# Optimization experiments

Hardware: AMD Instinct MI355X
Metric: run time of the kernel (lower is better)

The kernel has to match this reference:

```python
import jax, jax.numpy as jnp
import numpy as np

B, L, D = 2, 384, 128
N, DHS, DHP = 8, 16, 4  # heads, scalar head dim, point head dim
D_SCALAR = N * DHS          # 128
D_POINT = N * DHP * 3       # 96
D_OUT_IN = D_SCALAR + D * N + D_POINT + N * DHP  # 1280


def setup_inputs() -> dict:
    key = jax.random.key(0)
    ks = jax.random.split(key, 14)
    sc = 0.05
    x = jax.random.normal(ks[0], (B, L, D), dtype=jnp.float32)
    e = jax.random.normal(ks[1], (B, L, L, D), dtype=jnp.float32)
    r = jax.random.normal(ks[2], (B, L, 3, 3), dtype=jnp.float32)
    t = jax.random.normal(ks[3], (B, L, 3), dtype=jnp.float32)
    Wq_s = jax.random.normal(ks[4], (D, D_SCALAR)) * sc
    Wk_s = jax.random.normal(ks[5], (D, D_SCALAR)) * sc
    Wv_s = jax.random.normal(ks[6], (D, D_SCALAR)) * sc
    Wb = jax.random.normal(ks[7], (D, N)) * sc
    Wq_p = jax.random.normal(ks[8], (D, D_POINT)) * sc
    Wk_p = jax.random.normal(ks[9], (D, D_POINT)) * sc
    Wv_p = jax.random.normal(ks[10], (D, D_POINT)) * sc
    gamma = jnp.full((N,), float(np.log(np.exp(1.0) - 1.0)), dtype=jnp.float32)
    Wo = jax.random.normal(ks[11], (D_OUT_IN, D)) * sc
    bo = jnp.zeros((D,), dtype=jnp.float32)
    return {"x": x, "e": e, "r": r, "t": t, "Wq_s": Wq_s, "Wk_s": Wk_s,
            "Wv_s": Wv_s, "Wb": Wb, "Wq_p": Wq_p, "Wk_p": Wk_p,
            "Wv_p": Wv_p, "gamma": gamma, "Wo": Wo, "bo": bo}


def _heads_scalar(y):  # (b,l,n*d) -> (b,n,l,d)
    b, l, _ = y.shape
    return y.reshape(b, l, N, DHS).transpose(0, 2, 1, 3)


def _heads_point(y):  # (b,l,n*p*3) -> (b,n,l,p,3)
    b, l, _ = y.shape
    return y.reshape(b, l, N, DHP, 3).transpose(0, 2, 1, 3, 4)


def reference(x, e, r, t, Wq_s, Wk_s, Wv_s, Wb, Wq_p, Wk_p, Wv_p, gamma, Wo, bo):
    b, l, _ = x.shape
    qs = _heads_scalar(x @ Wq_s)
    ks_ = _heads_scalar(x @ Wk_s)
    vs = _heads_scalar(x @ Wv_s)

    # local points -> global frame: x_row @ r + t (note row-vector convention)
    t_b = t[:, None, :, None, :]  # (b,1,l,1,3)
    qp = jnp.einsum('bnlpk,blkc->bnlpc', _heads_point(x @ Wq_p), r) + t_b
    kp = jnp.einsum('bnlpk,blkc->bnlpc', _heads_point(x @ Wk_p), r) + t_b
    vp = jnp.einsum('bnlpk,blkc->bnlpc', _heads_point(x @ Wv_p), r) + t_b

    logit_scalar = jnp.einsum('bnid,bnjd->bnij', qs, ks_) * (DHS ** -0.5)
    bias_pair = jnp.einsum('bijd,dn->bnij', e, Wb)

    # sum_{p,c} (q_i - k_j)^2 via norm expansion (same math, no O(l^2 p 3) tensor)
    qq = jnp.sum(qp * qp, axis=(-1, -2))  # (b,n,i)
    kk = jnp.sum(kp * kp, axis=(-1, -2))  # (b,n,j)
    cross = jnp.einsum('bnipc,bnjpc->bnij', qp, kp)
    dist2 = qq[..., :, None] + kk[..., None, :] - 2.0 * cross
    logit_point = (-0.5 * 0.25) * gamma[None, :, None, None] * dist2

    logit = (3.0 ** -0.5) * (logit_scalar + bias_pair + logit_point)
    attn = jax.nn.softmax(logit, axis=-1)  # (b,n,i,j)

    out_scalar = jnp.einsum('bnij,bnjd->bnid', attn, vs)
    out_scalar = out_scalar.transpose(0, 2, 1, 3).reshape(b, l, N * DHS)

    out_pair = jnp.einsum('bnij,bijd->bnid', attn, e)
    out_pair = out_pair.transpose(0, 2, 1, 3).reshape(b, l, N * D)

    op = jnp.einsum('bnij,bnjpc->bnipc', attn, vp)
    # inverse transform: (x - t) @ r^T  -> out[c] = sum_k (x-t)[k] * r[c,k]
    op_local = jnp.einsum('bnipk,bick->bnipc', op - t_b, r)
    op_norm = jnp.linalg.norm(op_local, axis=-1)  # (b,n,i,p)

    out_point = op_local.transpose(0, 2, 1, 3, 4).reshape(b, l, N * DHP * 3)
    out_norm = op_norm.transpose(0, 2, 1, 3).reshape(b, l, N * DHP)

    out = jnp.concatenate([out_scalar, out_pair, out_point, out_norm], axis=-1)
    return out @ Wo + bo
```

## Files before the change

kernel.cpp:

```cpp
#include <hip/hip_runtime.h>

#define LL 384
#define NH 8

typedef const float* fp32p;

__global__ __launch_bounds__(128) void k_proj(
    fp32p x, fp32p r, fp32p tvec,
    fp32p Wqs, fp32p Wks, fp32p Wvs,
    fp32p Wqp, fp32p Wkp, fp32p Wvp,
    float* qs, float* ks, float* vs,
    float* qp, float* kp, float* vp)
{
  int bl = blockIdx.x;
  int t = threadIdx.x;
  __shared__ float xs[128];
  __shared__ float yq[96], yk[96], yv[96];
  xs[t] = x[bl*128 + t];
  __syncthreads();
  float aq = 0.f, ak = 0.f, av = 0.f;
  #pragma unroll 4
  for (int d = 0; d < 128; ++d) {
    float xv = xs[d];
    aq += xv * Wqs[d*128 + t];
    ak += xv * Wks[d*128 + t];
    av += xv * Wvs[d*128 + t];
  }
  int b = bl / LL, l = bl - (bl / LL) * LL;
  int n = t >> 4, dhs = t & 15;
  int rowbase = (b*NH + n)*LL + l;
  qs[rowbase*16 + dhs] = aq;
  ks[rowbase*16 + dhs] = ak;
  vs[rowbase*16 + dhs] = av;
  if (t < 96) {
    float pq = 0.f, pk = 0.f, pv = 0.f;
    #pragma unroll 4
    for (int d = 0; d < 128; ++d) {
      float xv = xs[d];
      pq += xv * Wqp[d*96 + t];
      pk += xv * Wkp[d*96 + t];
      pv += xv * Wvp[d*96 + t];
    }
    yq[t] = pq; yk[t] = pk; yv[t] = pv;
  }
  __syncthreads();
  if (t < 96) {
    int np = t / 12;
    int rem = t - np*12;
    int p = rem / 3, c = rem - p*3;
    float rr0 = r[(bl*3 + 0)*3 + c];
    float rr1 = r[(bl*3 + 1)*3 + c];
    float rr2 = r[(bl*3 + 2)*3 + c];
    float tt  = tvec[bl*3 + c];
    int base = np*12 + p*3;
    int prow = (b*NH + np)*LL + l;
    qp[prow*12 + p*3 + c] = yq[base]*rr0 + yq[base+1]*rr1 + yq[base+2]*rr2 + tt;
    kp[prow*12 + p*3 + c] = yk[base]*rr0 + yk[base+1]*rr1 + yk[base+2]*rr2 + tt;
    vp[prow*12 + p*3 + c] = yv[base]*rr0 + yv[base+1]*rr1 + yv[base+2]*rr2 + tt;
  }
}

__global__ __launch_bounds__(256) void k_fused(
    fp32p e, fp32p Wb, fp32p gamma, fp32p r, fp32p tvec,
    const float* qs, const float* ks, const float* vs,
    const float* qp, const float* kp, const float* vp,
    float* cat)
{
  int bi = blockIdx.x;
  int b = bi / LL, i = bi - (bi / LL)*LL;
  int t = threadIdx.x;
  __shared__ float attnS[8*385];
  __shared__ float WbS[1024];
  __shared__ float qS[128];
  __shared__ float qpS[96];
  __shared__ float qqS[8], coefS[8];
  __shared__ float redS[128*9];
  __shared__ float opS[96];

  const float* ebase = e + (size_t)bi*LL*128;

  #pragma unroll
  for (int u = 0; u < 4; ++u) WbS[t + u*256] = Wb[t + u*256];
  if (t < 128) {
    int n = t >> 4, d = t & 15;
    qS[t] = qs[(size_t)(((b*NH + n)*LL + i))*16 + d];
  } else if (t < 224) {
    int tt = t - 128;
    int n = tt / 12, d = tt - n*12;
    qpS[tt] = qp[(size_t)(((b*NH + n)*LL + i))*12 + d];
  } else if (t < 232) {
    coefS[t - 224] = -0.125f * gamma[t - 224];
  }
  __syncthreads();

  if (t < 192) {
    const float4* er0 = reinterpret_cast<const float4*>(ebase + (size_t)t*128);
    const float4* er1 = reinterpret_cast<const float4*>(ebase + (size_t)(t + 192)*128);
    float acc0[8] = {0,0,0,0,0,0,0,0};
    float acc1[8] = {0,0,0,0,0,0,0,0};
    for (int d4 = 0; d4 < 32; ++d4) {
      float4 e0 = er0[d4], e1 = er1[d4];
      float a0[4] = {e0.x, e0.y, e0.z, e0.w};
      float a1[4] = {e1.x, e1.y, e1.z, e1.w};
      #pragma unroll
      for (int k = 0; k < 4; ++k) {
        int d = d4*4 + k;
        float4 w0 = *reinterpret_cast<const float4*>(&WbS[d*8]);
        float4 w1 = *reinterpret_cast<const float4*>(&WbS[d*8 + 4]);
        acc0[0] += a0[k]*w0.x; acc0[1] += a0[k]*w0.y; acc0[2] += a0[k]*w0.z; acc0[3] += a0[k]*w0.w;
        acc0[4] += a0[k]*w1.x; acc0[5] += a0[k]*w1.y; acc0[6] += a0[k]*w1.z; acc0[7] += a0[k]*w1.w;
        acc1[0] += a1[k]*w0.x; acc1[1] += a1[k]*w0.y; acc1[2] += a1[k]*w0.z; acc1[3] += a1[k]*w0.w;
        acc1[4] += a1[k]*w1.x; acc1[5] += a1[k]*w1.y; acc1[6] += a1[k]*w1.z; acc1[7] += a1[k]*w1.w;
      }
    }
    #pragma unroll
    for (int n = 0; n < 8; ++n) {
      attnS[n*385 + t]       = acc0[n];
      attnS[n*385 + t + 192] = acc1[n];
    }
  } else if (t < 200) {
    int n = t - 192;
    float s = 0.f;
    #pragma unroll
    for (int k = 0; k < 12; ++k) { float v = qpS[n*12 + k]; s += v*v; }
    qqS[n] = s;
  }
  __syncthreads();

  if (t < 192) {
    #pragma unroll
    for (int n = 0; n < 8; ++n) {
      int bn = b*NH + n;
      float4 q0 = *reinterpret_cast<const float4*>(&qS[n*16]);
      float4 q1 = *reinterpret_cast<const float4*>(&qS[n*16 + 4]);
      float4 q2 = *reinterpret_cast<const float4*>(&qS[n*16 + 8]);
      float4 q3 = *reinterpret_cast<const float4*>(&qS[n*16 + 12]);
      float4 p0 = *reinterpret_cast<const float4*>(&qpS[n*12]);
      float4 p1 = *reinterpret_cast<const float4*>(&qpS[n*12 + 4]);
      float4 p2 = *reinterpret_cast<const float4*>(&qpS[n*12 + 8]);
      float qq = qqS[n], coef = coefS[n];
      #pragma unroll
      for (int jj = 0; jj < 2; ++jj) {
        int j = t + jj*192;
        size_t rowk = (size_t)bn*LL + j;
        const float4* k4  = reinterpret_cast<const float4*>(ks + rowk*16);
        const float4* kp4 = reinterpret_cast<const float4*>(kp + rowk*12);
        float4 k0 = k4[0], k1 = k4[1], k2 = k4[2], k3 = k4[3];
        float dots = q0.x*k0.x + q0.y*k0.y + q0.z*k0.z + q0.w*k0.w
                   + q1.x*k1.x + q1.y*k1.y + q1.z*k1.z + q1.w*k1.w
                   + q2.x*k2.x + q2.y*k2.y + q2.z*k2.z + q2.w*k2.w
                   + q3.x*k3.x + q3.y*k3.y + q3.z*k3.z + q3.w*k3.w;
        float4 c0 = kp4[0], c1 = kp4[1], c2 = kp4[2];
        float cross = p0.x*c0.x + p0.y*c0.y + p0.z*c0.z + p0.w*c0.w
                    + p1.x*c1.x + p1.y*c1.y + p1.z*c1.z + p1.w*c1.w
                    + p2.x*c2.x + p2.y*c2.y + p2.z*c2.z + p2.w*c2.w;
        float kk = c0.x*c0.x + c0.y*c0.y + c0.z*c0.z + c0.w*c0.w
                 + c1.x*c1.x + c1.y*c1.y + c1.z*c1.z + c1.w*c1.w
                 + c2.x*c2.x + c2.y*c2.y + c2.z*c2.z + c2.w*c2.w;
        float bs = attnS[n*385 + j];
        attnS[n*385 + j] = 0.57735027f * (0.25f*dots + bs + coef*(qq + kk - 2.f*cross));
      }
    }
  }
  __syncthreads();

  {
    int wv = t >> 6, lane = t & 63;
    #pragma unroll
    for (int nn2 = 0; nn2 < 2; ++nn2) {
      int n = wv*2 + nn2;
      float v[6];
      #pragma unroll
      for (int q = 0; q < 6; ++q) v[q] = attnS[n*385 + lane + q*64];
      float m = v[0];
      #pragma unroll
      for (int q = 1; q < 6; ++q) m = fmaxf(m, v[q]);
      #pragma unroll
      for (int off = 32; off >= 1; off >>= 1) m = fmaxf(m, __shfl_xor(m, off, 64));
      float s = 0.f;
      #pragma unroll
      for (int q = 0; q < 6; ++q) { v[q] = __expf(v[q] - m); s += v[q]; }
      #pragma unroll
      for (int off = 32; off >= 1; off >>= 1) s += __shfl_xor(s, off, 64);
      float inv = 1.f / s;
      #pragma unroll
      for (int q = 0; q < 6; ++q) attnS[n*385 + lane + q*64] = v[q]*inv;
    }
  }
  __syncthreads();

  if (t < 224) {
    int n = t / 28, d = t - (t / 28)*28;
    const float* an = attnS + n*385;
    size_t rowbase = (size_t)(b*NH + n)*LL;
    float acc = 0.f;
    if (d < 16) {
      const float* src = vs + rowbase*16 + d;
      for (int j = 0; j < LL; ++j) acc += an[j] * src[j*16];
      cat[(size_t)bi*1280 + n*16 + d] = acc;
    } else {
      const float* src = vp + rowbase*12 + (d - 16);
      for (int j = 0; j < LL; ++j) acc += an[j] * src[j*12];
      opS[n*12 + (d - 16)] = acc;
    }
  }
  __syncthreads();

  {
    int oct = t & 15, n3 = (t >> 4) & 7, half = t >> 7;
    const float* an = attnS + n3*385;
    const float4* e4 = reinterpret_cast<const float4*>(ebase);
    float acc[8] = {0,0,0,0,0,0,0,0};
    for (int jj = 0; jj < 192; ++jj) {
      int j = 2*jj + half;
      float4 va = e4[j*32 + oct*2];
      float4 vb = e4[j*32 + oct*2 + 1];
      float a = an[j];
      acc[0] += a*va.x; acc[1] += a*va.y; acc[2] += a*va.z; acc[3] += a*va.w;
      acc[4] += a*vb.x; acc[5] += a*vb.y; acc[6] += a*vb.z; acc[7] += a*vb.w;
    }
    if (half) {
      #pragma unroll
      for (int k = 0; k < 8; ++k) redS[(t - 128)*9 + k] = acc[k];
    }
    __syncthreads();
    if (!half) {
      float* dst = cat + (size_t)bi*1280 + 128 + n3*128 + oct*8;
      #pragma unroll
      for (int k = 0; k < 8; ++k) dst[k] = acc[k] + redS[t*9 + k];
    }
  }

  if (t < 32) {
    int n = t >> 2, p = t & 3;
    float o[3];
    #pragma unroll
    for (int k = 0; k < 3; ++k) o[k] = opS[n*12 + p*3 + k] - tvec[bi*3 + k];
    float loc[3];
    #pragma unroll
    for (int c = 0; c < 3; ++c) {
      float s = 0.f;
      #pragma unroll
      for (int k = 0; k < 3; ++k) s += o[k] * r[(bi*3 + c)*3 + k];
      loc[c] = s;
    }
    float* dst = cat + (size_t)bi*1280;
    dst[1152 + n*12 + p*3 + 0] = loc[0];
    dst[1152 + n*12 + p*3 + 1] = loc[1];
    dst[1152 + n*12 + p*3 + 2] = loc[2];
    dst[1248 + n*4 + p] = sqrtf(loc[0]*loc[0] + loc[1]*loc[1] + loc[2]*loc[2]);
  }
}

__global__ __launch_bounds__(256) void k_out(const float* cat, fp32p Wo, fp32p bo,
                                             float* out)
{
  int r0 = blockIdx.x * 8;
  int t = threadIdx.x;
  __shared__ float catS[8*1280];
  {
    const float4* c4 = reinterpret_cast<const float4*>(cat + (size_t)r0*1280);
    float4* s4 = reinterpret_cast<float4*>(catS);
    for (int idx = t; idx < 2560; idx += 256) s4[idx] = c4[idx];
  }
  __syncthreads();
  int row = t >> 5;
  int cg  = t & 31;
  const float* crow = catS + row*1280;
  const float4* w4 = reinterpret_cast<const float4*>(Wo) + cg;
  float ax = 0.f, ay = 0.f, az = 0.f, aw = 0.f;
  for (int k = 0; k < 1280; k += 16) {
    float4 w[16]; float a[16];
    #pragma unroll
    for (int u = 0; u < 16; ++u) { w[u] = w4[(k + u)*32]; a[u] = crow[k + u]; }
    #pragma unroll
    for (int u = 0; u < 16; ++u) {
      ax += a[u]*w[u].x; ay += a[u]*w[u].y; az += a[u]*w[u].z; aw += a[u]*w[u].w;
    }
  }
  float4 bv = reinterpret_cast<const float4*>(bo)[cg];
  float4 res = { ax + bv.x, ay + bv.y, az + bv.z, aw + bv.w };
  reinterpret_cast<float4*>(out + (size_t)(r0 + row)*128)[cg] = res;
}

extern "C" void kernel_launch(void* const* d_in, const int* in_sizes, int n_in,
                              void* d_out, int out_size, void* d_ws, size_t ws_size,
                              hipStream_t stream)
{
  fp32p x    = (fp32p)d_in[0];
  fp32p e    = (fp32p)d_in[1];
  fp32p r    = (fp32p)d_in[2];
  fp32p tv   = (fp32p)d_in[3];
  fp32p Wqs  = (fp32p)d_in[4];
  fp32p Wks  = (fp32p)d_in[5];
  fp32p Wvs  = (fp32p)d_in[6];
  fp32p Wb   = (fp32p)d_in[7];
  fp32p Wqp  = (fp32p)d_in[8];
  fp32p Wkp  = (fp32p)d_in[9];
  fp32p Wvp  = (fp32p)d_in[10];
  fp32p gam  = (fp32p)d_in[11];
  fp32p Wo   = (fp32p)d_in[12];
  fp32p bo   = (fp32p)d_in[13];
  float* out = (float*)d_out;

  float* qs  = (float*)d_ws;
  float* ks  = qs + 98304;
  float* vs  = ks + 98304;
  float* qp  = vs + 98304;
  float* kp  = qp + 73728;
  float* vp  = kp + 73728;
  float* cat = vp + 73728;

  k_proj<<<768, 128, 0, stream>>>(x, r, tv, Wqs, Wks, Wvs, Wqp, Wkp, Wvp,
                                  qs, ks, vs, qp, kp, vp);
  k_fused<<<768, 256, 0, stream>>>(e, Wb, gam, r, tv, qs, ks, vs, qp, kp, vp, cat);
  k_out<<<96, 256, 0, stream>>>(cat, Wo, bo, out);
}
```

Measured before the change: 439.7 us.

## Split fused attention kernel into logit, softmax, AV, pair and point kernels

The monolithic per-row kernel is broken into separate kernels for the logits, softmax, attention-times-values, the pair aggregation over the edge tensor, and the point back-transform. Attention weights now round-trip through a global buffer, and the pair aggregation is split four ways along j, with results combined by atomic adds into a pre-zeroed output buffer. The aim is more parallelism and occupancy than 768 heavy blocks using large shared memory could offer. The cost is extra launches, about 9 MB of attention-matrix traffic and float atomics, while the 75 MB edge tensor is still read twice.

```diff
diff --git a/kernel.cpp b/kernel.cpp
--- a/kernel.cpp
+++ b/kernel.cpp
@@ -4,6 +4,11 @@
 #define NH 8
 
 typedef const float* fp32p;
+
+__global__ __launch_bounds__(256) void k_zero(float4* p)
+{
+  p[(size_t)blockIdx.x*256 + threadIdx.x] = make_float4(0.f, 0.f, 0.f, 0.f);
+}
 
 __global__ __launch_bounds__(128) void k_proj(
     fp32p x, fp32p r, fp32p tvec,
@@ -19,7 +24,6 @@
   xs[t] = x[bl*128 + t];
   __syncthreads();
   float aq = 0.f, ak = 0.f, av = 0.f;
-  #pragma unroll 4
   for (int d = 0; d < 128; ++d) {
     float xv = xs[d];
     aq += xv * Wqs[d*128 + t];
@@ -34,7 +38,6 @@
   vs[rowbase*16 + dhs] = av;
   if (t < 96) {
     float pq = 0.f, pk = 0.f, pv = 0.f;
-    #pragma unroll 4
     for (int d = 0; d < 128; ++d) {
       float xv = xs[d];
       pq += xv * Wqp[d*96 + t];
@@ -60,196 +63,174 @@
   }
 }
 
-__global__ __launch_bounds__(256) void k_fused(
-    fp32p e, fp32p Wb, fp32p gamma, fp32p r, fp32p tvec,
-    const float* qs, const float* ks, const float* vs,
-    const float* qp, const float* kp, const float* vp,
-    float* cat)
-{
-  int bi = blockIdx.x;
+__global__ __launch_bounds__(256) void k_logit(
+    fp32p e, fp32p Wb, fp32p gamma,
+    const float* qs, const float* ks, const float* qp, const float* kp,
+    float* attn)
+{
+  __shared__ float WbS[1024];
+  int t = threadIdx.x;
+  #pragma unroll
+  for (int u = 0; u < 4; ++u) WbS[t + u*256] = Wb[t + u*256];
+  __syncthreads();
+  int gtid = blockIdx.x*256 + t;
+  int bi = gtid / 192, j0 = gtid - (gtid / 192)*192;
+  int b = bi / LL, i = bi - (bi / LL)*LL;
+  const float4* er0 = reinterpret_cast<const float4*>(e + ((size_t)bi*LL + j0)*128);
+  const float4* er1 = reinterpret_cast<const float4*>(e + ((size_t)bi*LL + j0 + 192)*128);
+  float acc0[8] = {0,0,0,0,0,0,0,0};
+  float acc1[8] = {0,0,0,0,0,0,0,0};
+  for (int d4 = 0; d4 < 32; ++d4) {
+    float4 e0 = er0[d4], e1 = er1[d4];
+    float a0[4] = {e0.x, e0.y, e0.z, e0.w};
+    float a1[4] = {e1.x, e1.y, e1.z, e1.w};
+    #pragma unroll
+    for (int k = 0; k < 4; ++k) {
+      int d = d4*4 + k;
+      float4 w0 = *reinterpret_cast<const float4*>(&WbS[d*8]);
+      float4 w1 = *reinterpret_cast<const float4*>(&WbS[d*8 + 4]);
+      acc0[0] += a0[k]*w0.x; acc0[1] += a0[k]*w0.y; acc0[2] += a0[k]*w0.z; acc0[3] += a0[k]*w0.w;
+      acc0[4] += a0[k]*w1.x; acc0[5] += a0[k]*w1.y; acc0[6] += a0[k]*w1.z; acc0[7] += a0[k]*w1.w;
+      acc1[0] += a1[k]*w0.x; acc1[1] += a1[k]*w0.y; acc1[2] += a1[k]*w0.z; acc1[3] += a1[k]*w0.w;
+      acc1[4] += a1[k]*w1.x; acc1[5] += a1[k]*w1.y; acc1[6] += a1[k]*w1.z; acc1[7] += a1[k]*w1.w;
+    }
+  }
+  #pragma unroll
+  for (int n = 0; n < 8; ++n) {
+    size_t rq = (size_t)(b*NH + n)*LL + i;
+    const float4* q4 = reinterpret_cast<const float4*>(qs + rq*16);
+    float4 q0 = q4[0], q1 = q4[1], q2 = q4[2], q3 = q4[3];
+    const float4* p4 = reinterpret_cast<const float4*>(qp + rq*12);
+    float4 p0 = p4[0], p1 = p4[1], p2 = p4[2];
+    float qq = p0.x*p0.x + p0.y*p0.y + p0.z*p0.z + p0.w*p0.w
+             + p1.x*p1.x + p1.y*p1.y + p1.z*p1.z + p1.w*p1.w
+             + p2.x*p2.x + p2.y*p2.y + p2.z*p2.z + p2.w*p2.w;
+    float coef = -0.125f * gamma[n];
+    #pragma unroll
+    for (int jj = 0; jj < 2; ++jj) {
+      int j = j0 + jj*192;
+      size_t rk = (size_t)(b*NH + n)*LL + j;
+      const float4* k4  = reinterpret_cast<const float4*>(ks + rk*16);
+      const float4* kp4 = reinterpret_cast<const float4*>(kp + rk*12);
+      float4 k0 = k4[0], k1 = k4[1], k2 = k4[2], k3 = k4[3];
+      float dots = q0.x*k0.x + q0.y*k0.y + q0.z*k0.z + q0.w*k0.w
+                 + q1.x*k1.x + q1.y*k1.y + q1.z*k1.z + q1.w*k1.w
+                 + q2.x*k2.x + q2.y*k2.y + q2.z*k2.z + q2.w*k2.w
+                 + q3.x*k3.x + q3.y*k3.y + q3.z*k3.z + q3.w*k3.w;
+      float4 c0 = kp4[0], c1 = kp4[1], c2 = kp4[2];
+      float cross = p0.x*c0.x + p0.y*c0.y + p0.z*c0.z + p0.w*c0.w
+                  + p1.x*c1.x + p1.y*c1.y + p1.z*c1.z + p1.w*c1.w
+                  + p2.x*c2.x + p2.y*c2.y + p2.z*c2.z + p2.w*c2.w;
+      float kk = c0.x*c0.x + c0.y*c0.y + c0.z*c0.z + c0.w*c0.w
+               + c1.x*c1.x + c1.y*c1.y + c1.z*c1.z + c1.w*c1.w
+               + c2.x*c2.x + c2.y*c2.y + c2.z*c2.z + c2.w*c2.w;
+      float bias = jj ? acc1[n] : acc0[n];
+      attn[((size_t)(b*NH + n)*LL + i)*LL + j] =
+          0.57735027f * (0.25f*dots + bias + coef*(qq + kk - 2.f*cross));
+    }
+  }
+}
+
+__global__ __launch_bounds__(256) void k_soft(float* attn)
+{
+  int row = blockIdx.x*4 + (threadIdx.x >> 6);
+  int lane = threadIdx.x & 63;
+  float* arow = attn + (size_t)row*LL;
+  float v[6];
+  #pragma unroll
+  for (int q = 0; q < 6; ++q) v[q] = arow[lane + q*64];
+  float m = v[0];
+  #pragma unroll
+  for (int q = 1; q < 6; ++q) m = fmaxf(m, v[q]);
+  #pragma unroll
+  for (int off = 32; off >= 1; off >>= 1) m = fmaxf(m, __shfl_xor(m, off, 64));
+  float s = 0.f;
+  #pragma unroll
+  for (int q = 0; q < 6; ++q) { v[q] = __expf(v[q] - m); s += v[q]; }
+  #pragma unroll
+  for (int off = 32; off >= 1; off >>= 1) s += __shfl_xor(s, off, 64);
+  float inv = 1.f / s;
+  #pragma unroll
+  for (int q = 0; q < 6; ++q) arow[lane + q*64] = v[q]*inv;
+}
+
+__global__ __launch_bounds__(256) void k_av(
+    const float* attn, const float* vs, const float* vp, float* cat, float* opb)
+{
+  int tid = blockIdx.x*256 + threadIdx.x;
+  int row = tid >> 5;
+  int dim = tid & 31;
+  if (dim >= 28) return;
+  int i = row % LL;
+  int bn = row / LL;
+  int rowbase = bn * LL;
+  const float* arow = attn + (size_t)row*LL;
+  const float* src; int stride;
+  if (dim < 16) { src = vs + (size_t)rowbase*16 + dim; stride = 16; }
+  else          { src = vp + (size_t)rowbase*12 + (dim - 16); stride = 12; }
+  float acc = 0.f;
+  for (int j = 0; j < LL; ++j) acc += arow[j] * src[(size_t)j*stride];
+  int b = bn >> 3, n = bn & 7;
+  if (dim < 16) cat[((size_t)(b*LL + i))*1280 + n*16 + dim] = acc;
+  else          opb[(size_t)row*12 + (dim - 16)] = acc;
+}
+
+__global__ __launch_bounds__(256) void k_pair(fp32p e, const float* attn, float* cat)
+{
+  int blk = blockIdx.x;
+  int bi = blk >> 2, s = blk & 3;
   int b = bi / LL, i = bi - (bi / LL)*LL;
   int t = threadIdx.x;
-  __shared__ float attnS[8*385];
-  __shared__ float WbS[1024];
-  __shared__ float qS[128];
-  __shared__ float qpS[96];
-  __shared__ float qqS[8], coefS[8];
-  __shared__ float redS[128*9];
-  __shared__ float opS[96];
-
-  const float* ebase = e + (size_t)bi*LL*128;
-
-  #pragma unroll
-  for (int u = 0; u < 4; ++u) WbS[t + u*256] = Wb[t + u*256];
-  if (t < 128) {
-    int n = t >> 4, d = t & 15;
-    qS[t] = qs[(size_t)(((b*NH + n)*LL + i))*16 + d];
-  } else if (t < 224) {
-    int tt = t - 128;
-    int n = tt / 12, d = tt - n*12;
-    qpS[tt] = qp[(size_t)(((b*NH + n)*LL + i))*12 + d];
-  } else if (t < 232) {
-    coefS[t - 224] = -0.125f * gamma[t - 224];
-  }
-  __syncthreads();
-
-  if (t < 192) {
-    const float4* er0 = reinterpret_cast<const float4*>(ebase + (size_t)t*128);
-    const float4* er1 = reinterpret_cast<const float4*>(ebase + (size_t)(t + 192)*128);
-    float acc0[8] = {0,0,0,0,0,0,0,0};
-    float acc1[8] = {0,0,0,0,0,0,0,0};
-    for (int d4 = 0; d4 < 32; ++d4) {
-      float4 e0 = er0[d4], e1 = er1[d4];
-      float a0[4] = {e0.x, e0.y, e0.z, e0.w};
-      float a1[4] = {e1.x, e1.y, e1.z, e1.w};
-      #pragma unroll
-      for (int k = 0; k < 4; ++k) {
-        int d = d4*4 + k;
-        float4 w0 = *reinterpret_cast<const float4*>(&WbS[d*8]);
-        float4 w1 = *reinterpret_cast<const float4*>(&WbS[d*8 + 4]);
-        acc0[0] += a0[k]*w0.x; acc0[1] += a0[k]*w0.y; acc0[2] += a0[k]*w0.z; acc0[3] += a0[k]*w0.w;
-        acc0[4] += a0[k]*w1.x; acc0[5] += a0[k]*w1.y; acc0[6] += a0[k]*w1.z; acc0[7] += a0[k]*w1.w;
-        acc1[0] += a1[k]*w0.x; acc1[1] += a1[k]*w0.y; acc1[2] += a1[k]*w0.z; acc1[3] += a1[k]*w0.w;
-        acc1[4] += a1[k]*w1.x; acc1[5] += a1[k]*w1.y; acc1[6] += a1[k]*w1.z; acc1[7] += a1[k]*w1.w;
-      }
-    }
-    #pragma unroll
-    for (int n = 0; n < 8; ++n) {
-      attnS[n*385 + t]       = acc0[n];
-      attnS[n*385 + t + 192] = acc1[n];
-    }
-  } else if (t < 200) {
-    int n = t - 192;
+  __shared__ float attnS[768];
+  #pragma unroll
+  for (int u = 0; u < 3; ++u) {
+    int idx = t + u*256;
+    int n2 = idx / 96, jj = idx - n2*96;
+    attnS[idx] = attn[((size_t)(b*NH + n2)*LL + i)*LL + s*96 + jj];
+  }
+  __syncthreads();
+  int n = t >> 5, d4 = t & 31;
+  const float4* e4 = reinterpret_cast<const float4*>(e) + ((size_t)bi*LL + s*96)*32 + d4;
+  const float* an = attnS + n*96;
+  float4 acc = make_float4(0.f, 0.f, 0.f, 0.f);
+  for (int jj = 0; jj < 96; ++jj) {
+    float4 ev = e4[(size_t)jj*32];
+    float a = an[jj];
+    acc.x += a*ev.x; acc.y += a*ev.y; acc.z += a*ev.z; acc.w += a*ev.w;
+  }
+  float* dst = cat + (size_t)bi*1280 + 128 + n*128 + d4*4;
+  atomicAdd(dst + 0, acc.x);
+  atomicAdd(dst + 1, acc.y);
+  atomicAdd(dst + 2, acc.z);
+  atomicAdd(dst + 3, acc.w);
+}
+
+__global__ __launch_bounds__(256) void k_pt(const float* opb, fp32p r, fp32p tvec, float* cat)
+{
+  int tid = blockIdx.x*256 + threadIdx.x;
+  int p = tid & 3;
+  int row = tid >> 2;
+  int i = row % LL;
+  int bn = row / LL;
+  int b = bn >> 3, n = bn & 7;
+  int bi = b*LL + i;
+  float o[3];
+  #pragma unroll
+  for (int k = 0; k < 3; ++k)
+    o[k] = opb[(size_t)row*12 + p*3 + k] - tvec[bi*3 + k];
+  float loc[3];
+  #pragma unroll
+  for (int c = 0; c < 3; ++c) {
     float s = 0.f;
     #pragma unroll
-    for (int k = 0; k < 12; ++k) { float v = qpS[n*12 + k]; s += v*v; }
-    qqS[n] = s;
-  }
-  __syncthreads();
-
-  if (t < 192) {
-    #pragma unroll
-    for (int n = 0; n < 8; ++n) {
-      int bn = b*NH + n;
-      float4 q0 = *reinterpret_cast<const float4*>(&qS[n*16]);
-      float4 q1 = *reinterpret_cast<const float4*>(&qS[n*16 + 4]);
-      float4 q2 = *reinterpret_cast<const float4*>(&qS[n*16 + 8]);
-      float4 q3 = *reinterpret_cast<const float4*>(&qS[n*16 + 12]);
-      float4 p0 = *reinterpret_cast<const float4*>(&qpS[n*12]);
-      float4 p1 = *reinterpret_cast<const float4*>(&qpS[n*12 + 4]);
-      float4 p2 = *reinterpret_cast<const float4*>(&qpS[n*12 + 8]);
-      float qq = qqS[n], coef = coefS[n];
-      #pragma unroll
-      for (int jj = 0; jj < 2; ++jj) {
-        int j = t + jj*192;
-        size_t rowk = (size_t)bn*LL + j;
-        const float4* k4  = reinterpret_cast<const float4*>(ks + rowk*16);
-        const float4* kp4 = reinterpret_cast<const float4*>(kp + rowk*12);
-        float4 k0 = k4[0], k1 = k4[1], k2 = k4[2], k3 = k4[3];
-        float dots = q0.x*k0.x + q0.y*k0.y + q0.z*k0.z + q0.w*k0.w
-                   + q1.x*k1.x + q1.y*k1.y + q1.z*k1.z + q1.w*k1.w
-                   + q2.x*k2.x + q2.y*k2.y + q2.z*k2.z + q2.w*k2.w
-                   + q3.x*k3.x + q3.y*k3.y + q3.z*k3.z + q3.w*k3.w;
-        float4 c0 = kp4[0], c1 = kp4[1], c2 = kp4[2];
-        float cross = p0.x*c0.x + p0.y*c0.y + p0.z*c0.z + p0.w*c0.w
-                    + p1.x*c1.x + p1.y*c1.y + p1.z*c1.z + p1.w*c1.w
-                    + p2.x*c2.x + p2.y*c2.y + p2.z*c2.z + p2.w*c2.w;
-        float kk = c0.x*c0.x + c0.y*c0.y + c0.z*c0.z + c0.w*c0.w
-                 + c1.x*c1.x + c1.y*c1.y + c1.z*c1.z + c1.w*c1.w
-                 + c2.x*c2.x + c2.y*c2.y + c2.z*c2.z + c2.w*c2.w;
-        float bs = attnS[n*385 + j];
-        attnS[n*385 + j] = 0.57735027f * (0.25f*dots + bs + coef*(qq + kk - 2.f*cross));
-      }
-    }
-  }
-  __syncthreads();
-
-  {
-    int wv = t >> 6, lane = t & 63;
-    #pragma unroll
-    for (int nn2 = 0; nn2 < 2; ++nn2) {
-      int n = wv*2 + nn2;
-      float v[6];
-      #pragma unroll
-      for (int q = 0; q < 6; ++q) v[q] = attnS[n*385 + lane + q*64];
-      float m = v[0];
-      #pragma unroll
-      for (int q = 1; q < 6; ++q) m = fmaxf(m, v[q]);
-      #pragma unroll
-      for (int off = 32; off >= 1; off >>= 1) m = fmaxf(m, __shfl_xor(m, off, 64));
-      float s = 0.f;
-      #pragma unroll
-      for (int q = 0; q < 6; ++q) { v[q] = __expf(v[q] - m); s += v[q]; }
-      #pragma unroll
-      for (int off = 32; off >= 1; off >>= 1) s += __shfl_xor(s, off, 64);
-      float inv = 1.f / s;
-      #pragma unroll
-      for (int q = 0; q < 6; ++q) attnS[n*385 + lane + q*64] = v[q]*inv;
-    }
-  }
-  __syncthreads();
-
-  if (t < 224) {
-    int n = t / 28, d = t - (t / 28)*28;
-    const float* an = attnS + n*385;
-    size_t rowbase = (size_t)(b*NH + n)*LL;
-    float acc = 0.f;
-    if (d < 16) {
-      const float* src = vs + rowbase*16 + d;
-      for (int j = 0; j < LL; ++j) acc += an[j] * src[j*16];
-      cat[(size_t)bi*1280 + n*16 + d] = acc;
-    } else {
-      const float* src = vp + rowbase*12 + (d - 16);
-      for (int j = 0; j < LL; ++j) acc += an[j] * src[j*12];
-      opS[n*12 + (d - 16)] = acc;
-    }
-  }
-  __syncthreads();
-
-  {
-    int oct = t & 15, n3 = (t >> 4) & 7, half = t >> 7;
-    const float* an = attnS + n3*385;
-    const float4* e4 = reinterpret_cast<const float4*>(ebase);
-    float acc[8] = {0,0,0,0,0,0,0,0};
-    for (int jj = 0; jj < 192; ++jj) {
-      int j = 2*jj + half;
-      float4 va = e4[j*32 + oct*2];
-      float4 vb = e4[j*32 + oct*2 + 1];
-      float a = an[j];
-      acc[0] += a*va.x; acc[1] += a*va.y; acc[2] += a*va.z; acc[3] += a*va.w;
-      acc[4] += a*vb.x; acc[5] += a*vb.y; acc[6] += a*vb.z; acc[7] += a*vb.w;
-    }
-    if (half) {
-      #pragma unroll
-      for (int k = 0; k < 8; ++k) redS[(t - 128)*9 + k] = acc[k];
-    }
-    __syncthreads();
-    if (!half) {
-      float* dst = cat + (size_t)bi*1280 + 128 + n3*128 + oct*8;
-      #pragma unroll
-      for (int k = 0; k < 8; ++k) dst[k] = acc[k] + redS[t*9 + k];
-    }
-  }
-
-  if (t < 32) {
-    int n = t >> 2, p = t & 3;
-    float o[3];
-    #pragma unroll
-    for (int k = 0; k < 3; ++k) o[k] = opS[n*12 + p*3 + k] - tvec[bi*3 + k];
-    float loc[3];
-    #pragma unroll
-    for (int c = 0; c < 3; ++c) {
-      float s = 0.f;
-      #pragma unroll
-      for (int k = 0; k < 3; ++k) s += o[k] * r[(bi*3 + c)*3 + k];
-      loc[c] = s;
-    }
-    float* dst = cat + (size_t)bi*1280;
-    dst[1152 + n*12 + p*3 + 0] = loc[0];
-    dst[1152 + n*12 + p*3 + 1] = loc[1];
-    dst[1152 + n*12 + p*3 + 2] = loc[2];
-    dst[1248 + n*4 + p] = sqrtf(loc[0]*loc[0] + loc[1]*loc[1] + loc[2]*loc[2]);
-  }
+    for (int k = 0; k < 3; ++k) s += o[k] * r[(bi*3 + c)*3 + k];
+    loc[c] = s;
+  }
+  float* dst = cat + (size_t)bi*1280;
+  dst[1152 + n*12 + p*3 + 0] = loc[0];
+  dst[1152 + n*12 + p*3 + 1] = loc[1];
+  dst[1152 + n*12 + p*3 + 2] = loc[2];
+  dst[1248 + n*4 + p] = sqrtf(loc[0]*loc[0] + loc[1]*loc[1] + loc[2]*loc[2]);
 }
 
 __global__ __launch_bounds__(256) void k_out(const float* cat, fp32p Wo, fp32p bo,
@@ -303,16 +284,23 @@
   fp32p bo   = (fp32p)d_in[13];
   float* out = (float*)d_out;
 
-  float* qs  = (float*)d_ws;
-  float* ks  = qs + 98304;
-  float* vs  = ks + 98304;
-  float* qp  = vs + 98304;
-  float* kp  = qp + 73728;
-  float* vp  = kp + 73728;
-  float* cat = vp + 73728;
-
+  float* qs   = (float*)d_ws;
+  float* ks   = qs + 98304;
+  float* vs   = ks + 98304;
+  float* qp   = vs + 98304;
+  float* kp   = qp + 73728;
+  float* vp   = kp + 73728;
+  float* attn = vp + 73728;
+  float* opb  = attn + 2359296;
+  float* cat  = opb + 73728;
+
+  k_zero<<<960, 256, 0, stream>>>(reinterpret_cast<float4*>(cat));
   k_proj<<<768, 128, 0, stream>>>(x, r, tv, Wqs, Wks, Wvs, Wqp, Wkp, Wvp,
                                   qs, ks, vs, qp, kp, vp);
-  k_fused<<<768, 256, 0, stream>>>(e, Wb, gam, r, tv, qs, ks, vs, qp, kp, vp, cat);
+  k_logit<<<576, 256, 0, stream>>>(e, Wb, gam, qs, ks, qp, kp, attn);
+  k_soft<<<1536, 256, 0, stream>>>(attn);
+  k_av<<<768, 256, 0, stream>>>(attn, vs, vp, cat, opb);
+  k_pair<<<3072, 256, 0, stream>>>(e, attn, cat);
+  k_pt<<<96, 256, 0, stream>>>(opb, r, tv, cat);
   k_out<<<96, 256, 0, stream>>>(cat, Wo, bo, out);
 }
```

After: 445.7 us. About the same (+1.4%).
